# Kernel optimization log

Measured on AMD Instinct MI355X. Metric: run time of the kernel, lower is better.

## Reference

```python
import jax, jax.numpy as jnp
import numpy as np

N, E, M = 100000, 1600000, 10000
D_IN, D_HID, D_OUT = 128, 128, 128


def setup_inputs() -> dict:
    key = jax.random.key(0)
    ks = jax.random.split(key, 16)
    feat = jax.random.normal(ks[0], (N, D_IN), dtype=jnp.float32)
    src = jax.random.randint(ks[1], (E,), 0, N, dtype=jnp.int32)
    dst = jax.random.randint(ks[2], (E,), 0, N, dtype=jnp.int32)
    masked_offset = jax.random.randint(ks[3], (M,), 0, N, dtype=jnp.int32)
    def xavier(k, shape):
        fan_in, fan_out = shape[0], shape[1]
        a = jnp.sqrt(6.0 / (fan_in + fan_out))
        return jax.random.uniform(k, shape, jnp.float32, -a, a)
    return {
        'feat': feat, 'src': src, 'dst': dst, 'masked_offset': masked_offset,
        # GraphConv layers (weight [in,out], bias [out])
        'W1': xavier(ks[4], (D_IN, D_HID)), 'b1': jnp.zeros((D_HID,), jnp.float32),
        'W2': xavier(ks[5], (D_HID, D_HID)), 'b2': jnp.zeros((D_HID,), jnp.float32),
        # fusion MLP
        'Wm1': xavier(ks[6], (D_HID + D_IN, D_HID)), 'bm1': jnp.zeros((D_HID,), jnp.float32),
        'Wm2': xavier(ks[7], (D_HID, D_HID)), 'bm2': jnp.zeros((D_HID,), jnp.float32),
        'Wm3': xavier(ks[8], (D_HID, D_OUT)),  # final Linear has bias=False
    }


def _graph_conv_right(h, src, dst, W, b, inv_deg):
    # DGL GraphConv(norm='right'): aggregate src features at dst, divide by in-degree.
    # Apply weight first (in_feats >= out_feats path) -- mathematically identical.
    hw = h @ W                                   # [N, out]
    agg = jax.ops.segment_sum(hw[src], dst, num_segments=N)  # scatter-add over edges
    return agg * inv_deg + b


def reference(feat, src, dst, masked_offset, W1, b1, W2, b2, Wm1, bm1, Wm2, bm2, Wm3):
    ones = jnp.ones((E,), jnp.float32)
    deg = jax.ops.segment_sum(ones, dst, num_segments=N)
    inv_deg = (1.0 / jnp.clip(deg, 1.0, None))[:, None]      # [N,1]
    # GCN layer 1 + ReLU (Identity norm)
    h = jax.nn.relu(_graph_conv_right(feat, src, dst, W1, b1, inv_deg))
    # GCN layer 2 (last layer: no activation; dropout no-op at eval)
    h = _graph_conv_right(h, src, dst, W2, b2, inv_deg)
    # fusion == 'cat': relu(Identity(h[masked])) concat raw features
    hm = jax.nn.relu(h[masked_offset])                       # [M, H]
    x = jnp.concatenate([hm, feat[masked_offset]], axis=1)   # [M, H+D]
    x = jax.nn.relu(x @ Wm1 + bm1)
    x = jax.nn.relu(x @ Wm2 + bm2)
    return x @ Wm3
```

## Files before the change

### kernel.cpp

```cpp
#include <hip/hip_runtime.h>

#define NN 100000
#define NE 1600000
#define NM 10000
#define NSB 256
#define SUBN 391
#define CAP2 7424
#define PCH 2048

typedef __attribute__((ext_vector_type(8))) short bf16x8;
typedef __attribute__((ext_vector_type(4))) float f32x4;

__device__ inline float4 ld4(const float* p) { return *(const float4*)p; }
__device__ inline float bf2f(unsigned short u) {
  union { unsigned int i; float f; } c; c.i = ((unsigned int)u) << 16; return c.f;
}
__device__ inline unsigned short f2bf(float f) {
  union { float f; unsigned int i; } c; c.f = f;
  unsigned int u = c.i + 0x7fffu + ((c.i >> 16) & 1u);
  return (unsigned short)(u >> 16);
}
__device__ inline void stx(unsigned char* base, int rowBytes, int row, int col,
                           unsigned short val) {
  int bc = col * 2;
  int c = bc >> 4, cp = c ^ (row & 15);
  *(unsigned short*)&base[row * rowBytes + (cp << 4) + (bc & 15)] = val;
}
__device__ inline bf16x8 ldx8(const unsigned char* base, int rowBytes, int row, int kc) {
  return *(const bf16x8*)&base[row * rowBytes + ((kc ^ (row & 15)) << 4)];
}

__global__ __launch_bounds__(256) void part2_k(const int* __restrict__ src,
                                               const int* __restrict__ dst,
                                               unsigned* __restrict__ parts2,
                                               int* __restrict__ pcnt2) {
  __shared__ int cntw[4][NSB];
  __shared__ int basew[4][NSB];
  __shared__ int bstart[NSB + 1];
  __shared__ int gbase[NSB];
  __shared__ int wsum[4];
  __shared__ unsigned buf[PCH];
  __shared__ unsigned char bb[PCH];
  const int tid = threadIdx.x;
  const int wv = tid >> 6;
  const int e0 = blockIdx.x * PCH;

  for (int i = tid; i < 4 * NSB; i += 256) ((int*)cntw)[i] = 0;
  __syncthreads();

  unsigned pk[8];
  int b_[8], lp_[8];
#pragma unroll
  for (int j = 0; j < 8; ++j) {
    int e = e0 + j * 256 + tid;
    bool ok = e < NE;
    int s = ok ? src[e] : 0;
    int d = ok ? dst[e] : 0;
    int b = d / SUBN;
    int ld = d - b * SUBN;
    pk[j] = ((unsigned)ld << 17) | (unsigned)s;
    b_[j] = ok ? b : -1;
    if (ok) lp_[j] = atomicAdd(&cntw[wv][b], 1);
  }
  __syncthreads();
  int t0 = cntw[0][tid], t1 = cntw[1][tid], t2 = cntw[2][tid], t3 = cntw[3][tid];
  int tot = t0 + t1 + t2 + t3;
  int x = tot;
#pragma unroll
  for (int d = 1; d < 64; d <<= 1) {
    int y = __shfl_up(x, d, 64);
    if ((tid & 63) >= d) x += y;
  }
  if ((tid & 63) == 63) wsum[wv] = x;
  __syncthreads();
  int woff = 0;
#pragma unroll
  for (int w = 0; w < 4; ++w) woff += (w < wv) ? wsum[w] : 0;
  int excl = x + woff - tot;
  bstart[tid] = excl;
  basew[0][tid] = excl;
  basew[1][tid] = excl + t0;
  basew[2][tid] = excl + t0 + t1;
  basew[3][tid] = excl + t0 + t1 + t2;
  gbase[tid] = atomicAdd(&pcnt2[tid], tot);
  if (tid == NSB - 1) bstart[NSB] = excl + tot;
  __syncthreads();
#pragma unroll
  for (int j = 0; j < 8; ++j)
    if (b_[j] >= 0) {
      int pos = basew[wv][b_[j]] + lp_[j];
      buf[pos] = pk[j];
      bb[pos] = (unsigned char)b_[j];
    }
  __syncthreads();
  int total = bstart[NSB];
  for (int i = tid; i < total; i += 256) {
    int b = bb[i];
    int gi = gbase[b] + (i - bstart[b]);
    if (gi < CAP2) parts2[(size_t)b * CAP2 + gi] = buf[i];
  }
}

__global__ __launch_bounds__(1024) void deg2_k(const unsigned* __restrict__ parts2,
                                               const int* __restrict__ pcnt2,
                                               int* __restrict__ deg) {
  __shared__ int cnt[SUBN];
  int sb = blockIdx.x;
  int n = min(pcnt2[sb], CAP2);
  const unsigned* p = parts2 + (size_t)sb * CAP2;
  for (int i = threadIdx.x; i < SUBN; i += 1024) cnt[i] = 0;
  __syncthreads();
  for (int i = threadIdx.x; i < n; i += 1024) atomicAdd(&cnt[p[i] >> 17], 1);
  __syncthreads();
  int base = sb * SUBN;
  for (int i = threadIdx.x; i < SUBN; i += 1024)
    if (base + i < NN) deg[base + i] = cnt[i];
}

__global__ __launch_bounds__(1024) void scan1_k(const int* __restrict__ deg,
                                                int* __restrict__ excl,
                                                int* __restrict__ bsum, int n) {
  __shared__ int lds[1024];
  int tid = threadIdx.x;
  int gid = blockIdx.x * 1024 + tid;
  int v = (gid < n) ? deg[gid] : 0;
  lds[tid] = v;
  __syncthreads();
  for (int off = 1; off < 1024; off <<= 1) {
    int t = (tid >= off) ? lds[tid - off] : 0;
    __syncthreads();
    lds[tid] += t;
    __syncthreads();
  }
  if (gid < n) excl[gid] = lds[tid] - v;
  if (tid == 1023) bsum[blockIdx.x] = lds[1023];
}

__global__ void scan2_k(int* __restrict__ bsum, int nb) {
  __shared__ int lds[128];
  int tid = threadIdx.x;
  int v = (tid < nb) ? bsum[tid] : 0;
  lds[tid] = v;
  __syncthreads();
  for (int off = 1; off < 128; off <<= 1) {
    int t = (tid >= off) ? lds[tid - off] : 0;
    __syncthreads();
    lds[tid] += t;
    __syncthreads();
  }
  if (tid < nb) bsum[tid] = lds[tid] - v;
}

__global__ __launch_bounds__(256) void scan3_k(int* __restrict__ excl,
                                               const int* __restrict__ bsum,
                                               const int* __restrict__ deg,
                                               float* __restrict__ inv, int n) {
  int gid = blockIdx.x * 256 + threadIdx.x;
  if (gid < n) {
    excl[gid] += bsum[gid >> 10] + deg[gid];
    inv[gid] = 1.0f / fmaxf((float)deg[gid], 1.0f);
  }
}

__global__ __launch_bounds__(1024) void sort_emit_k(const unsigned* __restrict__ parts2,
                                                    const int* __restrict__ pcnt2,
                                                    const int* __restrict__ offs_end,
                                                    const int* __restrict__ degv,
                                                    int* __restrict__ csr) {
  __shared__ int cur[SUBN];
  __shared__ int sorted[CAP2];
  int sb = blockIdx.x;
  int n = min(pcnt2[sb], CAP2);
  const unsigned* p = parts2 + (size_t)sb * CAP2;
  int base = sb * SUBN;
  int segbase = offs_end[base] - degv[base];
  for (int i = threadIdx.x; i < SUBN; i += 1024) {
    int nd = base + i;
    cur[i] = (nd < NN) ? (offs_end[nd] - degv[nd]) : 0;
  }
  __syncthreads();
  for (int i = threadIdx.x; i < n; i += 1024) {
    unsigned v = p[i];
    int pos = atomicAdd(&cur[v >> 17], 1);
    sorted[pos - segbase] = (int)(v & 0x1FFFFu);
  }
  __syncthreads();
  for (int i = threadIdx.x; i < n; i += 1024) csr[segbase + i] = sorted[i];
}

__global__ __launch_bounds__(256) void tobf_k(const float* __restrict__ x,
                                              unsigned short* __restrict__ y, int n) {
  int idx = (blockIdx.x * 256 + threadIdx.x) * 4;
  if (idx < n) {
    float4 v = ld4(x + idx);
    unsigned int lo = (unsigned int)f2bf(v.x) | ((unsigned int)f2bf(v.y) << 16);
    unsigned int hi = (unsigned int)f2bf(v.z) | ((unsigned int)f2bf(v.w) << 16);
    *(uint2*)(y + idx) = make_uint2(lo, hi);
  }
}

__device__ inline void convfrag(const float* W, unsigned short* Wf, int g) {
  int k8 = (g >> 7) << 3, col = g & 127;
  unsigned short tmp[8];
#pragma unroll
  for (int i = 0; i < 8; ++i) tmp[i] = f2bf(W[(k8 + i) * 128 + col]);
  *(uint4*)&Wf[(size_t)g * 8] = *(const uint4*)tmp;
}
__global__ __launch_bounds__(256) void wconv_k(const float* W1, const float* W2,
                                               const float* Wm1, const float* Wm2,
                                               const float* Wm3,
                                               unsigned short* W1f, unsigned short* W2f,
                                               unsigned short* Wm1f, unsigned short* Wm2f,
                                               unsigned short* Wm3f) {
  int g = blockIdx.x * 256 + threadIdx.x;
  if (g < 2048) convfrag(W1, W1f, g);
  else if (g < 4096) convfrag(W2, W2f, g - 2048);
  else if (g < 8192) convfrag(Wm1, Wm1f, g - 4096);
  else if (g < 10240) convfrag(Wm2, Wm2f, g - 8192);
  else if (g < 12288) convfrag(Wm3, Wm3f, g - 10240);
}

__global__ __launch_bounds__(256) void mark_k(const int* __restrict__ masked,
                                              const int* __restrict__ csr,
                                              const int* __restrict__ offs_end,
                                              const int* __restrict__ degv,
                                              unsigned char* __restrict__ needed) {
  int m = blockIdx.x * 8 + (threadIdx.x >> 5);
  if (m >= NM) return;
  int lane = threadIdx.x & 31;
  int v = masked[m];
  int cnt = degv[v];
  int start = offs_end[v] - cnt;
  for (int i = lane; i < cnt; i += 32) needed[csr[start + i]] = 1;
}

__global__ __launch_bounds__(256) void gather1_k(const unsigned short* __restrict__ featbf,
                                                 const int* __restrict__ csr,
                                                 const int* __restrict__ offs_end,
                                                 const int* __restrict__ degv,
                                                 const float* __restrict__ inv,
                                                 const unsigned char* __restrict__ needed,
                                                 unsigned short* __restrict__ agg1) {
  int v = blockIdx.x * 8 + (threadIdx.x >> 5);
  if (v >= NN) return;
  if (!needed[v]) return;
  int lane = threadIdx.x & 31;
  int cnt = degv[v];
  int start = offs_end[v] - cnt;
  const uint2* fb = (const uint2*)featbf;
  float a0 = 0.f, a1 = 0.f, a2 = 0.f, a3 = 0.f;
  int nb8 = (cnt + 7) >> 3;
  for (int it = 0; it < nb8; ++it) {
    int b = start + (it << 3);
    int rem = cnt - (it << 3);
    int sidx[8];
#pragma unroll
    for (int j = 0; j < 8; ++j) {
      int s = csr[b + (j < rem ? j : 0)];
      sidx[j] = (j < rem) ? s : NN;
    }
    uint2 x[8];
#pragma unroll
    for (int j = 0; j < 8; ++j) x[j] = fb[(size_t)sidx[j] * 32 + lane];
#pragma unroll
    for (int j = 0; j < 8; ++j) {
      a0 += bf2f((unsigned short)(x[j].x));
      a1 += bf2f((unsigned short)(x[j].x >> 16));
      a2 += bf2f((unsigned short)(x[j].y));
      a3 += bf2f((unsigned short)(x[j].y >> 16));
    }
  }
  float iv = inv[v];
  unsigned int lo = (unsigned int)f2bf(a0 * iv) | ((unsigned int)f2bf(a1 * iv) << 16);
  unsigned int hi = (unsigned int)f2bf(a2 * iv) | ((unsigned int)f2bf(a3 * iv) << 16);
  ((uint2*)agg1)[(size_t)v * 32 + lane] = make_uint2(lo, hi);
}

__global__ __launch_bounds__(256) void mfma1_k(const unsigned short* __restrict__ agg1,
                                               const unsigned short* __restrict__ W1f,
                                               const float* __restrict__ b1,
                                               unsigned short* __restrict__ h1bf) {
  const int tid = threadIdx.x;
  const int wave = tid >> 6, lane = tid & 63, l15 = lane & 15, l4 = lane >> 4;
  const int rbase = blockIdx.x * 64;
  int col0 = wave * 16 + l15, col1 = (wave + 4) * 16 + l15;
  bf16x8 Bfr0[4], Bfr1[4];
#pragma unroll
  for (int kt = 0; kt < 4; ++kt) {
    int kc = kt * 4 + l4;
    Bfr0[kt] = *(const bf16x8*)&W1f[((size_t)kc * 128 + col0) * 8];
    Bfr1[kt] = *(const bf16x8*)&W1f[((size_t)kc * 128 + col1) * 8];
  }
  float bias0 = b1[col0], bias1 = b1[col1];
  for (int rsub = 0; rsub < 4; ++rsub) {
    int arow = rbase + rsub * 16 + l15;
    const unsigned short* ap = agg1 + (size_t)min(arow, NN - 1) * 128;
    f32x4 acc0 = {0.f, 0.f, 0.f, 0.f};
    f32x4 acc1 = {0.f, 0.f, 0.f, 0.f};
#pragma unroll
    for (int kt = 0; kt < 4; ++kt) {
      int kc = kt * 4 + l4;
      bf16x8 a = *(const bf16x8*)(ap + kc * 8);
      acc0 = __builtin_amdgcn_mfma_f32_16x16x32_bf16(a, Bfr0[kt], acc0, 0, 0, 0);
      acc1 = __builtin_amdgcn_mfma_f32_16x16x32_bf16(a, Bfr1[kt], acc1, 0, 0, 0);
    }
#pragma unroll
    for (int r = 0; r < 4; ++r) {
      int orow = rbase + rsub * 16 + l4 * 4 + r;
      if (orow < NN) {
        h1bf[(size_t)orow * 128 + col0] = f2bf(fmaxf(acc0[r] + bias0, 0.f));
        h1bf[(size_t)orow * 128 + col1] = f2bf(fmaxf(acc1[r] + bias1, 0.f));
      }
    }
  }
}

__global__ __launch_bounds__(256) void gather2_k(const unsigned short* __restrict__ h1bf,
                                                 const int* __restrict__ masked,
                                                 const int* __restrict__ csr,
                                                 const int* __restrict__ offs_end,
                                                 const int* __restrict__ degv,
                                                 const float* __restrict__ inv,
                                                 unsigned short* __restrict__ agg2bf) {
  int m = blockIdx.x * 8 + (threadIdx.x >> 5);
  if (m >= NM) return;
  int lane = threadIdx.x & 31;
  int v = masked[m];
  int cnt = degv[v];
  int start = offs_end[v] - cnt;
  const uint2* fb = (const uint2*)h1bf;
  float a0 = 0.f, a1 = 0.f, a2 = 0.f, a3 = 0.f;
  int nb8 = (cnt + 7) >> 3;
  for (int it = 0; it < nb8; ++it) {
    int b = start + (it << 3);
    int rem = cnt - (it << 3);
    int sidx[8];
#pragma unroll
    for (int j = 0; j < 8; ++j) {
      int s = csr[b + (j < rem ? j : 0)];
      sidx[j] = (j < rem) ? s : NN;
    }
    uint2 x[8];
#pragma unroll
    for (int j = 0; j < 8; ++j) x[j] = fb[(size_t)sidx[j] * 32 + lane];
#pragma unroll
    for (int j = 0; j < 8; ++j) {
      a0 += bf2f((unsigned short)(x[j].x));
      a1 += bf2f((unsigned short)(x[j].x >> 16));
      a2 += bf2f((unsigned short)(x[j].y));
      a3 += bf2f((unsigned short)(x[j].y >> 16));
    }
  }
  float iv = inv[v];
  unsigned int lo = (unsigned int)f2bf(a0 * iv) | ((unsigned int)f2bf(a1 * iv) << 16);
  unsigned int hi = (unsigned int)f2bf(a2 * iv) | ((unsigned int)f2bf(a3 * iv) << 16);
  ((uint2*)agg2bf)[(size_t)m * 32 + lane] = make_uint2(lo, hi);
}

__global__ __launch_bounds__(256) void mlp_fused_k(const unsigned short* __restrict__ agg2bf,
                                                   const unsigned short* __restrict__ featbf,
                                                   const int* __restrict__ masked,
                                                   const unsigned short* __restrict__ W2f,
                                                   const float* __restrict__ b2,
                                                   const unsigned short* __restrict__ Wm1f,
                                                   const float* __restrict__ bm1,
                                                   const unsigned short* __restrict__ Wm2f,
                                                   const float* __restrict__ bm2,
                                                   const unsigned short* __restrict__ Wm3f,
                                                   float* __restrict__ out) {
  __shared__ unsigned char ldsX[64 * 512];
  __shared__ unsigned char ldsY[64 * 256];
  const int tid = threadIdx.x;
  const int rbase = blockIdx.x * 64;
  const int wave = tid >> 6, lane = tid & 63, l15 = lane & 15, l4 = lane >> 4;
  {
    int grp = tid >> 5, ln = tid & 31;
    uint2 vals[8];
#pragma unroll
    for (int k = 0; k < 8; ++k) {
      int m = rbase + grp * 8 + k;
      vals[k] = make_uint2(0u, 0u);
      if (m < NM) {
        int v = masked[m];
        vals[k] = ((const uint2*)featbf)[(size_t)v * 32 + ln];
      }
    }
#pragma unroll
    for (int k = 0; k < 8; ++k) {
      int row = grp * 8 + k;
      int c = 16 + (ln >> 1);
      *(uint2*)&ldsX[row * 512 + ((c ^ (row & 15)) << 4) + (ln & 1) * 8] = vals[k];
    }
  }
  {
    int col0 = wave * 16 + l15, col1 = (wave + 4) * 16 + l15;
    float bias0 = b2[col0], bias1 = b2[col1];
    for (int rsub = 0; rsub < 4; ++rsub) {
      int arow = rbase + rsub * 16 + l15;
      const unsigned short* ap = agg2bf + (size_t)min(arow, NM - 1) * 128;
      f32x4 acc0 = {0.f, 0.f, 0.f, 0.f};
      f32x4 acc1 = {0.f, 0.f, 0.f, 0.f};
#pragma unroll
      for (int kt = 0; kt < 4; ++kt) {
        int kc = kt * 4 + l4;
        bf16x8 a = *(const bf16x8*)(ap + kc * 8);
        bf16x8 b0 = *(const bf16x8*)&W2f[((size_t)kc * 128 + col0) * 8];
        bf16x8 b1v = *(const bf16x8*)&W2f[((size_t)kc * 128 + col1) * 8];
        acc0 = __builtin_amdgcn_mfma_f32_16x16x32_bf16(a, b0, acc0, 0, 0, 0);
        acc1 = __builtin_amdgcn_mfma_f32_16x16x32_bf16(a, b1v, acc1, 0, 0, 0);
      }
#pragma unroll
      for (int r = 0; r < 4; ++r) {
        int row = rsub * 16 + l4 * 4 + r;
        stx(ldsX, 512, row, col0, f2bf(fmaxf(acc0[r] + bias0, 0.f)));
        stx(ldsX, 512, row, col1, f2bf(fmaxf(acc1[r] + bias1, 0.f)));
      }
    }
  }
  __syncthreads();
  {
    int col0 = wave * 16 + l15, col1 = (wave + 4) * 16 + l15;
    float bias0 = bm1[col0], bias1 = bm1[col1];
    for (int rsub = 0; rsub < 4; ++rsub) {
      int row = rsub * 16 + l15;
      f32x4 acc0 = {0.f, 0.f, 0.f, 0.f};
      f32x4 acc1 = {0.f, 0.f, 0.f, 0.f};
#pragma unroll
      for (int kt = 0; kt < 8; ++kt) {
        int kc = kt * 4 + l4;
        bf16x8 a = ldx8(ldsX, 512, row, kc);
        bf16x8 b0 = *(const bf16x8*)&Wm1f[((size_t)kc * 128 + col0) * 8];
        bf16x8 b1v = *(const bf16x8*)&Wm1f[((size_t)kc * 128 + col1) * 8];
        acc0 = __builtin_amdgcn_mfma_f32_16x16x32_bf16(a, b0, acc0, 0, 0, 0);
        acc1 = __builtin_amdgcn_mfma_f32_16x16x32_bf16(a, b1v, acc1, 0, 0, 0);
      }
#pragma unroll
      for (int r = 0; r < 4; ++r) {
        int row2 = rsub * 16 + l4 * 4 + r;
        stx(ldsY, 256, row2, col0, f2bf(fmaxf(acc0[r] + bias0, 0.f)));
        stx(ldsY, 256, row2, col1, f2bf(fmaxf(acc1[r] + bias1, 0.f)));
      }
    }
  }
  __syncthreads();
  {
    int col0 = wave * 16 + l15, col1 = (wave + 4) * 16 + l15;
    float bias0 = bm2[col0], bias1 = bm2[col1];
    for (int rsub = 0; rsub < 4; ++rsub) {
      int row = rsub * 16 + l15;
      f32x4 acc0 = {0.f, 0.f, 0.f, 0.f};
      f32x4 acc1 = {0.f, 0.f, 0.f, 0.f};
#pragma unroll
      for (int kt = 0; kt < 4; ++kt) {
        int kc = kt * 4 + l4;
        bf16x8 a = ldx8(ldsY, 256, row, kc);
        bf16x8 b0 = *(const bf16x8*)&Wm2f[((size_t)kc * 128 + col0) * 8];
        bf16x8 b1v = *(const bf16x8*)&Wm2f[((size_t)kc * 128 + col1) * 8];
        acc0 = __builtin_amdgcn_mfma_f32_16x16x32_bf16(a, b0, acc0, 0, 0, 0);
        acc1 = __builtin_amdgcn_mfma_f32_16x16x32_bf16(a, b1v, acc1, 0, 0, 0);
      }
#pragma unroll
      for (int r = 0; r < 4; ++r) {
        int row2 = rsub * 16 + l4 * 4 + r;
        stx(ldsX, 256, row2, col0, f2bf(fmaxf(acc0[r] + bias0, 0.f)));
        stx(ldsX, 256, row2, col1, f2bf(fmaxf(acc1[r] + bias1, 0.f)));
      }
    }
  }
  __syncthreads();
  {
    int col0 = wave * 16 + l15, col1 = (wave + 4) * 16 + l15;
    for (int rsub = 0; rsub < 4; ++rsub) {
      int row = rsub * 16 + l15;
      f32x4 acc0 = {0.f, 0.f, 0.f, 0.f};
      f32x4 acc1 = {0.f, 0.f, 0.f, 0.f};
#pragma unroll
      for (int kt = 0; kt < 4; ++kt) {
        int kc = kt * 4 + l4;
        bf16x8 a = ldx8(ldsX, 256, row, kc);
        bf16x8 b0 = *(const bf16x8*)&Wm3f[((size_t)kc * 128 + col0) * 8];
        bf16x8 b1v = *(const bf16x8*)&Wm3f[((size_t)kc * 128 + col1) * 8];
        acc0 = __builtin_amdgcn_mfma_f32_16x16x32_bf16(a, b0, acc0, 0, 0, 0);
        acc1 = __builtin_amdgcn_mfma_f32_16x16x32_bf16(a, b1v, acc1, 0, 0, 0);
      }
#pragma unroll
      for (int r = 0; r < 4; ++r) {
        int orow = rbase + rsub * 16 + l4 * 4 + r;
        if (orow < NM) {
          out[(size_t)orow * 128 + col0] = acc0[r];
          out[(size_t)orow * 128 + col1] = acc1[r];
        }
      }
    }
  }
}

extern "C" void kernel_launch(void* const* d_in, const int* in_sizes, int n_in,
                              void* d_out, int out_size, void* d_ws, size_t ws_size,
                              hipStream_t stream) {
  const float* feat = (const float*)d_in[0];
  const int* src = (const int*)d_in[1];
  const int* dst = (const int*)d_in[2];
  const int* masked = (const int*)d_in[3];
  const float* W1 = (const float*)d_in[4];
  const float* b1 = (const float*)d_in[5];
  const float* W2 = (const float*)d_in[6];
  const float* b2 = (const float*)d_in[7];
  const float* Wm1 = (const float*)d_in[8];
  const float* bm1 = (const float*)d_in[9];
  const float* Wm2 = (const float*)d_in[10];
  const float* bm2 = (const float*)d_in[11];
  const float* Wm3 = (const float*)d_in[12];
  float* out = (float*)d_out;

  char* p = (char*)d_ws;
  int* deg = (int*)p;              p += (size_t)NN * 4;
  int* offs = (int*)p;             p += (size_t)NN * 4;
  int* bsum = (int*)p;             p += 128 * 4;
  int* pcnt2 = (int*)p;            p += NSB * 4;
  float* inv = (float*)p;          p += (size_t)NN * 4;
  int* csr = (int*)p;              p += (size_t)NE * 4;
  unsigned char* needed = (unsigned char*)p; p += (size_t)NN;
  p = (char*)(((size_t)p + 15) & ~(size_t)15);
  unsigned* parts2 = (unsigned*)p; p += (size_t)NSB * CAP2 * 4;
  unsigned short* featbf = (unsigned short*)p;  p += (size_t)(NN + 1) * 128 * 2;
  unsigned short* agg1 = (unsigned short*)p;    p += (size_t)NN * 128 * 2;
  unsigned short* h1bf = (unsigned short*)p;    p += (size_t)(NN + 1) * 128 * 2;
  unsigned short* agg2bf = (unsigned short*)p;  p += (size_t)NM * 128 * 2;
  unsigned short* W1f = (unsigned short*)p;     p += 16384 * 2;
  unsigned short* W2f = (unsigned short*)p;     p += 16384 * 2;
  unsigned short* Wm1f = (unsigned short*)p;    p += 32768 * 2;
  unsigned short* Wm2f = (unsigned short*)p;    p += 16384 * 2;
  unsigned short* Wm3f = (unsigned short*)p;    p += 16384 * 2;

  (void)hipMemsetAsync(pcnt2, 0, NSB * 4, stream);
  (void)hipMemsetAsync(needed, 0, NN, stream);
  (void)hipMemsetAsync(featbf + (size_t)NN * 128, 0, 256, stream);
  (void)hipMemsetAsync(h1bf + (size_t)NN * 128, 0, 256, stream);

  part2_k<<<(NE + PCH - 1) / PCH, 256, 0, stream>>>(src, dst, parts2, pcnt2);
  deg2_k<<<NSB, 1024, 0, stream>>>(parts2, pcnt2, deg);
  int nb = (NN + 1023) / 1024;
  scan1_k<<<nb, 1024, 0, stream>>>(deg, offs, bsum, NN);
  scan2_k<<<1, 128, 0, stream>>>(bsum, nb);
  scan3_k<<<(NN + 255) / 256, 256, 0, stream>>>(offs, bsum, deg, inv, NN);
  sort_emit_k<<<NSB, 1024, 0, stream>>>(parts2, pcnt2, offs, deg, csr);

  tobf_k<<<(NN * 128 / 4 + 255) / 256, 256, 0, stream>>>(feat, featbf, NN * 128);
  wconv_k<<<48, 256, 0, stream>>>(W1, W2, Wm1, Wm2, Wm3, W1f, W2f, Wm1f, Wm2f, Wm3f);

  mark_k<<<(NM + 7) / 8, 256, 0, stream>>>(masked, csr, offs, deg, needed);

  gather1_k<<<(NN + 7) / 8, 256, 0, stream>>>(featbf, csr, offs, deg, inv, needed, agg1);
  mfma1_k<<<(NN + 63) / 64, 256, 0, stream>>>(agg1, W1f, b1, h1bf);

  gather2_k<<<(NM + 7) / 8, 256, 0, stream>>>(h1bf, masked, csr, offs, deg, inv, agg2bf);

  mlp_fused_k<<<(NM + 63) / 64, 256, 0, stream>>>(agg2bf, featbf, masked,
                                                  W2f, b2, Wm1f, bm1, Wm2f, bm2, Wm3f, out);
}
```

Measured before the change: 185.1 us.

## Fuse front-end prep kernels into one launch and drop needed-node marking

Merges the edge partitioning, feature-to-bf16 conversion, weight fragment conversion and padding-row zeroing into a single block-dispatched kernel. This removes several launches and memsets and lets the independent jobs run concurrently. It also deletes the mark_k pass and the needed mask, so gather1 aggregates every node rather than only the neighbours of masked nodes. That saves the marking pass and memset but does extra gather work for nodes that are never used.

```diff
diff --git a/kernel.cpp b/kernel.cpp
--- a/kernel.cpp
+++ b/kernel.cpp
@@ -7,6 +7,9 @@
 #define SUBN 391
 #define CAP2 7424
 #define PCH 2048
+#define NBP2 782
+#define NBTB 1600
+#define NBWC 48
 
 typedef __attribute__((ext_vector_type(8))) short bf16x8;
 typedef __attribute__((ext_vector_type(4))) float f32x4;
@@ -30,10 +33,27 @@
   return *(const bf16x8*)&base[row * rowBytes + ((kc ^ (row & 15)) << 4)];
 }
 
-__global__ __launch_bounds__(256) void part2_k(const int* __restrict__ src,
+__device__ inline void convfrag(const float* W, unsigned short* Wf, int g) {
+  int k8 = (g >> 7) << 3, col = g & 127;
+  unsigned short tmp[8];
+#pragma unroll
+  for (int i = 0; i < 8; ++i) tmp[i] = f2bf(W[(k8 + i) * 128 + col]);
+  *(uint4*)&Wf[(size_t)g * 8] = *(const uint4*)tmp;
+}
+
+__global__ __launch_bounds__(256) void front_k(const int* __restrict__ src,
                                                const int* __restrict__ dst,
                                                unsigned* __restrict__ parts2,
-                                               int* __restrict__ pcnt2) {
+                                               int* __restrict__ pcnt2,
+                                               const float* __restrict__ feat,
+                                               unsigned short* __restrict__ featbf,
+                                               const float* W1, const float* W2,
+                                               const float* Wm1, const float* Wm2,
+                                               const float* Wm3,
+                                               unsigned short* W1f, unsigned short* W2f,
+                                               unsigned short* Wm1f, unsigned short* Wm2f,
+                                               unsigned short* Wm3f,
+                                               unsigned short* __restrict__ h1bf) {
   __shared__ int cntw[4][NSB];
   __shared__ int basew[4][NSB];
   __shared__ int bstart[NSB + 1];
@@ -41,63 +61,85 @@
   __shared__ int wsum[4];
   __shared__ unsigned buf[PCH];
   __shared__ unsigned char bb[PCH];
+  const int bid = blockIdx.x;
   const int tid = threadIdx.x;
-  const int wv = tid >> 6;
-  const int e0 = blockIdx.x * PCH;
-
-  for (int i = tid; i < 4 * NSB; i += 256) ((int*)cntw)[i] = 0;
-  __syncthreads();
-
-  unsigned pk[8];
-  int b_[8], lp_[8];
-#pragma unroll
-  for (int j = 0; j < 8; ++j) {
-    int e = e0 + j * 256 + tid;
-    bool ok = e < NE;
-    int s = ok ? src[e] : 0;
-    int d = ok ? dst[e] : 0;
-    int b = d / SUBN;
-    int ld = d - b * SUBN;
-    pk[j] = ((unsigned)ld << 17) | (unsigned)s;
-    b_[j] = ok ? b : -1;
-    if (ok) lp_[j] = atomicAdd(&cntw[wv][b], 1);
-  }
-  __syncthreads();
-  int t0 = cntw[0][tid], t1 = cntw[1][tid], t2 = cntw[2][tid], t3 = cntw[3][tid];
-  int tot = t0 + t1 + t2 + t3;
-  int x = tot;
-#pragma unroll
-  for (int d = 1; d < 64; d <<= 1) {
-    int y = __shfl_up(x, d, 64);
-    if ((tid & 63) >= d) x += y;
-  }
-  if ((tid & 63) == 63) wsum[wv] = x;
-  __syncthreads();
-  int woff = 0;
-#pragma unroll
-  for (int w = 0; w < 4; ++w) woff += (w < wv) ? wsum[w] : 0;
-  int excl = x + woff - tot;
-  bstart[tid] = excl;
-  basew[0][tid] = excl;
-  basew[1][tid] = excl + t0;
-  basew[2][tid] = excl + t0 + t1;
-  basew[3][tid] = excl + t0 + t1 + t2;
-  gbase[tid] = atomicAdd(&pcnt2[tid], tot);
-  if (tid == NSB - 1) bstart[NSB] = excl + tot;
-  __syncthreads();
-#pragma unroll
-  for (int j = 0; j < 8; ++j)
-    if (b_[j] >= 0) {
-      int pos = basew[wv][b_[j]] + lp_[j];
-      buf[pos] = pk[j];
-      bb[pos] = (unsigned char)b_[j];
-    }
-  __syncthreads();
-  int total = bstart[NSB];
-  for (int i = tid; i < total; i += 256) {
-    int b = bb[i];
-    int gi = gbase[b] + (i - bstart[b]);
-    if (gi < CAP2) parts2[(size_t)b * CAP2 + gi] = buf[i];
+
+  if (bid < NBP2) {
+    const int wv = tid >> 6;
+    const int e0 = bid * PCH;
+    for (int i = tid; i < 4 * NSB; i += 256) ((int*)cntw)[i] = 0;
+    __syncthreads();
+    unsigned pk[8];
+    int b_[8], lp_[8];
+#pragma unroll
+    for (int j = 0; j < 8; ++j) {
+      int e = e0 + j * 256 + tid;
+      bool ok = e < NE;
+      int s = ok ? src[e] : 0;
+      int d = ok ? dst[e] : 0;
+      int b = d / SUBN;
+      int ld = d - b * SUBN;
+      pk[j] = ((unsigned)ld << 17) | (unsigned)s;
+      b_[j] = ok ? b : -1;
+      if (ok) lp_[j] = atomicAdd(&cntw[wv][b], 1);
+    }
+    __syncthreads();
+    int t0 = cntw[0][tid], t1 = cntw[1][tid], t2 = cntw[2][tid], t3 = cntw[3][tid];
+    int tot = t0 + t1 + t2 + t3;
+    int x = tot;
+#pragma unroll
+    for (int d = 1; d < 64; d <<= 1) {
+      int y = __shfl_up(x, d, 64);
+      if ((tid & 63) >= d) x += y;
+    }
+    if ((tid & 63) == 63) wsum[wv] = x;
+    __syncthreads();
+    int woff = 0;
+#pragma unroll
+    for (int w = 0; w < 4; ++w) woff += (w < wv) ? wsum[w] : 0;
+    int excl = x + woff - tot;
+    bstart[tid] = excl;
+    basew[0][tid] = excl;
+    basew[1][tid] = excl + t0;
+    basew[2][tid] = excl + t0 + t1;
+    basew[3][tid] = excl + t0 + t1 + t2;
+    gbase[tid] = atomicAdd(&pcnt2[tid], tot);
+    if (tid == NSB - 1) bstart[NSB] = excl + tot;
+    __syncthreads();
+#pragma unroll
+    for (int j = 0; j < 8; ++j)
+      if (b_[j] >= 0) {
+        int pos = basew[wv][b_[j]] + lp_[j];
+        buf[pos] = pk[j];
+        bb[pos] = (unsigned char)b_[j];
+      }
+    __syncthreads();
+    int total = bstart[NSB];
+    for (int i = tid; i < total; i += 256) {
+      int b = bb[i];
+      int gi = gbase[b] + (i - bstart[b]);
+      if (gi < CAP2) parts2[(size_t)b * CAP2 + gi] = buf[i];
+    }
+  } else if (bid < NBP2 + NBTB) {
+    const int n4 = NN * 128 / 4;
+    for (int i = (bid - NBP2) * 256 + tid; i < n4; i += NBTB * 256) {
+      float4 v = ld4(feat + (size_t)i * 4);
+      unsigned int lo = (unsigned int)f2bf(v.x) | ((unsigned int)f2bf(v.y) << 16);
+      unsigned int hi = (unsigned int)f2bf(v.z) | ((unsigned int)f2bf(v.w) << 16);
+      ((uint2*)featbf)[i] = make_uint2(lo, hi);
+    }
+  } else if (bid < NBP2 + NBTB + NBWC) {
+    int g = (bid - NBP2 - NBTB) * 256 + tid;
+    if (g < 2048) convfrag(W1, W1f, g);
+    else if (g < 4096) convfrag(W2, W2f, g - 2048);
+    else if (g < 8192) convfrag(Wm1, Wm1f, g - 4096);
+    else if (g < 10240) convfrag(Wm2, Wm2f, g - 8192);
+    else if (g < 12288) convfrag(Wm3, Wm3f, g - 10240);
+  } else {
+    if (tid < 64) {
+      ((unsigned*)(featbf + (size_t)NN * 128))[tid] = 0u;
+      ((unsigned*)(h1bf + (size_t)NN * 128))[tid] = 0u;
+    }
   }
 }
 
@@ -188,62 +230,14 @@
   for (int i = threadIdx.x; i < n; i += 1024) csr[segbase + i] = sorted[i];
 }
 
-__global__ __launch_bounds__(256) void tobf_k(const float* __restrict__ x,
-                                              unsigned short* __restrict__ y, int n) {
-  int idx = (blockIdx.x * 256 + threadIdx.x) * 4;
-  if (idx < n) {
-    float4 v = ld4(x + idx);
-    unsigned int lo = (unsigned int)f2bf(v.x) | ((unsigned int)f2bf(v.y) << 16);
-    unsigned int hi = (unsigned int)f2bf(v.z) | ((unsigned int)f2bf(v.w) << 16);
-    *(uint2*)(y + idx) = make_uint2(lo, hi);
-  }
-}
-
-__device__ inline void convfrag(const float* W, unsigned short* Wf, int g) {
-  int k8 = (g >> 7) << 3, col = g & 127;
-  unsigned short tmp[8];
-#pragma unroll
-  for (int i = 0; i < 8; ++i) tmp[i] = f2bf(W[(k8 + i) * 128 + col]);
-  *(uint4*)&Wf[(size_t)g * 8] = *(const uint4*)tmp;
-}
-__global__ __launch_bounds__(256) void wconv_k(const float* W1, const float* W2,
-                                               const float* Wm1, const float* Wm2,
-                                               const float* Wm3,
-                                               unsigned short* W1f, unsigned short* W2f,
-                                               unsigned short* Wm1f, unsigned short* Wm2f,
-                                               unsigned short* Wm3f) {
-  int g = blockIdx.x * 256 + threadIdx.x;
-  if (g < 2048) convfrag(W1, W1f, g);
-  else if (g < 4096) convfrag(W2, W2f, g - 2048);
-  else if (g < 8192) convfrag(Wm1, Wm1f, g - 4096);
-  else if (g < 10240) convfrag(Wm2, Wm2f, g - 8192);
-  else if (g < 12288) convfrag(Wm3, Wm3f, g - 10240);
-}
-
-__global__ __launch_bounds__(256) void mark_k(const int* __restrict__ masked,
-                                              const int* __restrict__ csr,
-                                              const int* __restrict__ offs_end,
-                                              const int* __restrict__ degv,
-                                              unsigned char* __restrict__ needed) {
-  int m = blockIdx.x * 8 + (threadIdx.x >> 5);
-  if (m >= NM) return;
-  int lane = threadIdx.x & 31;
-  int v = masked[m];
-  int cnt = degv[v];
-  int start = offs_end[v] - cnt;
-  for (int i = lane; i < cnt; i += 32) needed[csr[start + i]] = 1;
-}
-
 __global__ __launch_bounds__(256) void gather1_k(const unsigned short* __restrict__ featbf,
                                                  const int* __restrict__ csr,
                                                  const int* __restrict__ offs_end,
                                                  const int* __restrict__ degv,
                                                  const float* __restrict__ inv,
-                                                 const unsigned char* __restrict__ needed,
                                                  unsigned short* __restrict__ agg1) {
   int v = blockIdx.x * 8 + (threadIdx.x >> 5);
   if (v >= NN) return;
-  if (!needed[v]) return;
   int lane = threadIdx.x & 31;
   int cnt = degv[v];
   int start = offs_end[v] - cnt;
@@ -520,7 +514,6 @@
   int* pcnt2 = (int*)p;            p += NSB * 4;
   float* inv = (float*)p;          p += (size_t)NN * 4;
   int* csr = (int*)p;              p += (size_t)NE * 4;
-  unsigned char* needed = (unsigned char*)p; p += (size_t)NN;
   p = (char*)(((size_t)p + 15) & ~(size_t)15);
   unsigned* parts2 = (unsigned*)p; p += (size_t)NSB * CAP2 * 4;
   unsigned short* featbf = (unsigned short*)p;  p += (size_t)(NN + 1) * 128 * 2;
@@ -534,11 +527,11 @@
   unsigned short* Wm3f = (unsigned short*)p;    p += 16384 * 2;
 
   (void)hipMemsetAsync(pcnt2, 0, NSB * 4, stream);
-  (void)hipMemsetAsync(needed, 0, NN, stream);
-  (void)hipMemsetAsync(featbf + (size_t)NN * 128, 0, 256, stream);
-  (void)hipMemsetAsync(h1bf + (size_t)NN * 128, 0, 256, stream);
-
-  part2_k<<<(NE + PCH - 1) / PCH, 256, 0, stream>>>(src, dst, parts2, pcnt2);
+
+  front_k<<<NBP2 + NBTB + NBWC + 1, 256, 0, stream>>>(
+      src, dst, parts2, pcnt2, feat, featbf,
+      W1, W2, Wm1, Wm2, Wm3, W1f, W2f, Wm1f, Wm2f, Wm3f, h1bf);
+
   deg2_k<<<NSB, 1024, 0, stream>>>(parts2, pcnt2, deg);
   int nb = (NN + 1023) / 1024;
   scan1_k<<<nb, 1024, 0, stream>>>(deg, offs, bsum, NN);
@@ -546,12 +539,7 @@
   scan3_k<<<(NN + 255) / 256, 256, 0, stream>>>(offs, bsum, deg, inv, NN);
   sort_emit_k<<<NSB, 1024, 0, stream>>>(parts2, pcnt2, offs, deg, csr);
 
-  tobf_k<<<(NN * 128 / 4 + 255) / 256, 256, 0, stream>>>(feat, featbf, NN * 128);
-  wconv_k<<<48, 256, 0, stream>>>(W1, W2, Wm1, Wm2, Wm3, W1f, W2f, Wm1f, Wm2f, Wm3f);
-
-  mark_k<<<(NM + 7) / 8, 256, 0, stream>>>(masked, csr, offs, deg, needed);
-
-  gather1_k<<<(NN + 7) / 8, 256, 0, stream>>>(featbf, csr, offs, deg, inv, needed, agg1);
+  gather1_k<<<(NN + 7) / 8, 256, 0, stream>>>(featbf, csr, offs, deg, inv, agg1);
   mfma1_k<<<(NN + 63) / 64, 256, 0, stream>>>(agg1, W1f, b1, h1bf);
 
   gather2_k<<<(NM + 7) / 8, 256, 0, stream>>>(h1bf, masked, csr, offs, deg, inv, agg2bf);
```

New measurement: 158.6 us. 14.3% less time.
